# Kernel tuning notes

Measured on AMD Instinct MI355X. Metric: run time of the kernel, lower is better.

Reference implementation:

```python
import jax, jax.numpy as jnp
import numpy as np

B, T0, J = 32, 2048, 128
C, T_L = 512, 16


def setup_inputs() -> dict:
    key = jax.random.key(0)
    k1, k2, k3, k4, k5 = jax.random.split(key, 5)
    x = jax.random.normal(k1, (B, T0, J), dtype=jnp.float32)
    lens = jax.random.randint(k2, (B,), 0, T0 - T_L)  # ensure idx stays in-range
    sos = jax.random.normal(k3, (J,), dtype=jnp.float32)
    label_seqs = jax.random.uniform(k4, (C, T_L, J), dtype=jnp.float32)
    W = jax.random.normal(k5, (J, J), dtype=jnp.float32) / np.sqrt(J)
    return {"x": x, "lens": lens, "sos": sos, "label_seqs": label_seqs, "W": W}


def _similarity(pred_seq, labels):
    # per-neuron squared-error similarity, averaged over J: [B,Tl,J],[C,Tl,J] -> [B,C,Tl]
    p2 = jnp.sum(pred_seq * pred_seq, axis=-1)          # [B,Tl]
    l2 = jnp.sum(labels * labels, axis=-1)              # [C,Tl]
    cross = jnp.einsum('btj,ctj->bct', pred_seq, labels)
    return (p2[:, None, :] + l2[None, :, :] - 2.0 * cross) / pred_seq.shape[-1]


def reference(x, lens, sos, label_seqs, W):
    b_ar = jnp.arange(B)
    sos_b = jnp.broadcast_to(sos, (B, J))
    # place sos at position lens[b], then prepend sos (vectorized scatter)
    x = x.at[b_ar, lens].set(sos_b)
    x = jnp.concatenate([sos_b[:, None, :], x], axis=1)  # [B, T0+1, J]
    idx2d = jnp.arange(T_L)[None, :] + lens[:, None] + 1  # [B, T_l]

    def gather_pred(xc):
        pred = jnp.einsum('btj,jk->btk', xc, W)          # stub search_forward
        return pred[b_ar[:, None], idx2d]                # [B, T_l, J]

    pls = gather_pred(x)
    sim0 = _similarity(pls[:, :1, :], label_seqs[:, :1, :])  # [B,C,1]
    sofar = jnp.argmin(sim0[:, :, 0], axis=-1)               # [B]

    def body(t, carry):
        xc, sofar, _ = carry
        lab = label_seqs[sofar]                              # [B, T_l, J]
        xc = xc.at[b_ar[:, None], idx2d].set(lab)            # fused scatter update
        pls = gather_pred(xc)
        sim = _similarity(pls, label_seqs)                   # [B, C, T_l]
        mask = (jnp.arange(T_L) < t).astype(sim.dtype)
        sim_mean = jnp.sum(sim * mask, axis=-1) / t
        sofar = jnp.argmin(sim_mean, axis=-1)
        return (xc, sofar, pls)

    _, sofar, pls = jax.lax.fori_loop(1, T_L + 1, body, (x, sofar, pls))
    return sofar, pls
```

## Files before the change

### kernel.cpp

```cpp
#include <hip/hip_runtime.h>

#define Jd   128
#define Cn   512
#define TLn  16
#define Bn   32


__device__ __forceinline__ unsigned int f2ord(float f) {
    unsigned int u = __float_as_uint(f);
    return (u & 0x80000000u) ? ~u : (u | 0x80000000u);
}
__device__ __forceinline__ unsigned long long packkey(float v, int c) {
    return ((unsigned long long)f2ord(v) << 32) | (unsigned int)c;
}

__global__ void __launch_bounds__(256, 4)
k_prep3(const float* __restrict__ L, const float* __restrict__ W,
        float* __restrict__ LT, float* __restrict__ l2T,
        float* __restrict__ PLT) {
    __shared__ float Lst[128][36];
    __shared__ float Ws[128][68];
    int tid = threadIdx.x, bid = blockIdx.x;
    int tau = bid & 15, jh = (bid >> 4) & 1, c0 = (bid >> 5) * 32;
    int j0 = jh * 64;

    int cr = tid >> 3, oc = tid & 7;
    const float4* src = (const float4*)(L + ((size_t)(c0 + cr) * TLn + tau) * Jd);
    float l2p = 0.f;
    #pragma unroll
    for (int i = 0; i < 4; ++i) {
        float4 v = src[oc * 4 + i];
        int kb = (oc * 4 + i) * 4;
        Lst[kb + 0][cr] = v.x;  Lst[kb + 1][cr] = v.y;
        Lst[kb + 2][cr] = v.z;  Lst[kb + 3][cr] = v.w;
        l2p += v.x * v.x + v.y * v.y + v.z * v.z + v.w * v.w;
    }
    l2p += __shfl_down(l2p, 4, 8);
    l2p += __shfl_down(l2p, 2, 8);
    l2p += __shfl_down(l2p, 1, 8);
    if (oc == 0 && jh == 0) l2T[tau * Cn + c0 + cr] = l2p;

    #pragma unroll
    for (int r = 0; r < 8; ++r) {
        int idx = r * 256 + tid;
        int k = idx >> 4, f = idx & 15;
        *(float4*)&Ws[k][f * 4] = *(const float4*)(W + (size_t)k * Jd + j0 + f * 4);
    }
    __syncthreads();

    int c = tid & 31, jq = tid >> 5;

    if (jh == 0) {
        #pragma unroll
        for (int k = jq; k < Jd; k += 8)
            LT[((size_t)tau * Jd + k) * Cn + c0 + c] = Lst[k][c];
    }

    float acc[8] = {};
    #pragma unroll 4
    for (int k = 0; k < Jd; ++k) {
        float a = Lst[k][c];
        float4 w0 = *(const float4*)&Ws[k][jq * 8];
        float4 w1 = *(const float4*)&Ws[k][jq * 8 + 4];
        acc[0] = fmaf(a, w0.x, acc[0]);
        acc[1] = fmaf(a, w0.y, acc[1]);
        acc[2] = fmaf(a, w0.z, acc[2]);
        acc[3] = fmaf(a, w0.w, acc[3]);
        acc[4] = fmaf(a, w1.x, acc[4]);
        acc[5] = fmaf(a, w1.y, acc[5]);
        acc[6] = fmaf(a, w1.z, acc[6]);
        acc[7] = fmaf(a, w1.w, acc[7]);
    }
    #pragma unroll
    for (int i = 0; i < 8; ++i)
        PLT[((size_t)tau * Jd + j0 + jq * 8 + i) * Cn + c0 + c] = acc[i];
}

__global__ void __launch_bounds__(256, 3)
k_dot(const float* __restrict__ LT, const float* __restrict__ PLT,
      const float* __restrict__ l2T,
      const float* __restrict__ sos, const float* __restrict__ W,
      float* __restrict__ DOT, float* __restrict__ S0) {
    __shared__ float As[64][64];
    __shared__ float Bs[64][128];
    int tid = threadIdx.x, bid = blockIdx.x;

    if (bid == 512) {
        float* pred0 = &As[0][0];
        if (tid < Jd) {
            float a = 0.f;
            for (int k = 0; k < Jd; ++k) a = fmaf(sos[k], W[k * Jd + tid], a);
            pred0[tid] = a;
        }
        __syncthreads();
        float a0 = 0.f, a1 = 0.f;
        for (int jj = 0; jj < Jd; ++jj) {
            float p = pred0[jj];
            float d0 = p - LT[(size_t)jj * Cn + tid];
            float d1 = p - LT[(size_t)jj * Cn + tid + 256];
            a0 = fmaf(d0, d0, a0);
            a1 = fmaf(d1, d1, a1);
        }
        S0[tid] = a0;  S0[tid + 256] = a1;
        return;
    }

    int tau = bid & 15, st = (bid >> 4) & 7, cq = bid >> 7;
    int s0 = st * 64, c0 = cq * 128;
    int sg = tid >> 4, cg = tid & 15;

    float acc[4][8] = {};
    for (int h = 0; h < 2; ++h) {
        __syncthreads();
        const float4* Asrc = (const float4*)(PLT + ((size_t)tau * Jd + h * 64) * Cn + s0);
        #pragma unroll
        for (int i = 0; i < 4; ++i) {
            int flat = i * 256 + tid;
            int row = flat >> 4, col = flat & 15;
            *(float4*)&As[row][col * 4] = Asrc[(size_t)row * (Cn / 4) + col];
        }
        const float4* Bsrc = (const float4*)(LT + ((size_t)tau * Jd + h * 64) * Cn + c0);
        #pragma unroll
        for (int i = 0; i < 8; ++i) {
            int flat = i * 256 + tid;
            int row = flat >> 5, col = flat & 31;
            *(float4*)&Bs[row][col * 4] = Bsrc[(size_t)row * (Cn / 4) + col];
        }
        __syncthreads();
        #pragma unroll 4
        for (int j = 0; j < 64; ++j) {
            float4 a  = *(const float4*)&As[j][sg * 4];
            float4 b0 = *(const float4*)&Bs[j][cg * 4];
            float4 b1 = *(const float4*)&Bs[j][64 + cg * 4];
            float av[4] = {a.x, a.y, a.z, a.w};
            float bv[8] = {b0.x, b0.y, b0.z, b0.w, b1.x, b1.y, b1.z, b1.w};
            #pragma unroll
            for (int i = 0; i < 4; ++i)
                #pragma unroll
                for (int q = 0; q < 8; ++q)
                    acc[i][q] = fmaf(av[i], bv[q], acc[i][q]);
        }
    }

    float4 l2a = *(const float4*)(l2T + tau * Cn + c0 + cg * 4);
    float4 l2b = *(const float4*)(l2T + tau * Cn + c0 + 64 + cg * 4);
    #pragma unroll
    for (int i = 0; i < 4; ++i) {
        int s = s0 + sg * 4 + i;
        float* dst = DOT + ((size_t)s * TLn + tau) * Cn + c0;
        float4 v0 = {l2a.x - 2.f * acc[i][0], l2a.y - 2.f * acc[i][1],
                     l2a.z - 2.f * acc[i][2], l2a.w - 2.f * acc[i][3]};
        float4 v1 = {l2b.x - 2.f * acc[i][4], l2b.y - 2.f * acc[i][5],
                     l2b.z - 2.f * acc[i][6], l2b.w - 2.f * acc[i][7]};
        *(float4*)(dst + cg * 4) = v0;
        *(float4*)(dst + 64 + cg * 4) = v1;
    }
}

__global__ void k_seq(const float* __restrict__ S0, const float* __restrict__ DOT,
                      int* __restrict__ keys) {
    __shared__ unsigned long long red[4];
    __shared__ int sCur;
    int tid = threadIdx.x, w = tid >> 6, lane = tid & 63;

    for (int t = 0; t <= TLn; ++t) {
        float sum0, sum1;
        if (t == 0) {
            sum0 = S0[tid];  sum1 = S0[tid + 256];
        } else {
            const float* base = DOT + (size_t)sCur * TLn * Cn;
            float v0[TLn], v1[TLn];
            #pragma unroll
            for (int tau = 0; tau < TLn; ++tau) {
                v0[tau] = base[(size_t)tau * Cn + tid];
                v1[tau] = base[(size_t)tau * Cn + tid + 256];
            }
            sum0 = sum1 = 0.f;
            #pragma unroll
            for (int tau = 0; tau < TLn; ++tau) {
                float m = (tau < t) ? 1.f : 0.f;
                sum0 = fmaf(v0[tau], m, sum0);
                sum1 = fmaf(v1[tau], m, sum1);
            }
        }
        unsigned long long m0 = packkey(sum0, tid);
        unsigned long long m1 = packkey(sum1, tid + 256);
        unsigned long long m = (m1 < m0) ? m1 : m0;
        for (int o = 32; o; o >>= 1) {
            unsigned long long o2 = __shfl_down(m, o, 64);
            if (o2 < m) m = o2;
        }
        if (lane == 0) red[w] = m;
        __syncthreads();
        if (tid == 0) {
            unsigned long long b = red[0];
            #pragma unroll
            for (int i = 1; i < 4; ++i) if (red[i] < b) b = red[i];
            int sv = (int)(b & 0xFFFFFFFFull);
            sCur = sv;  keys[t] = sv;
        }
        __syncthreads();
    }
}

__global__ void k_out(const float* __restrict__ PLT, const int* __restrict__ keys,
                      float* __restrict__ out) {
    int bt = blockIdx.x, j = threadIdx.x, tau = bt & (TLn - 1);
    int s16 = keys[TLn], s15 = keys[TLn - 1];
    out[Bn + (size_t)bt * Jd + j] = PLT[((size_t)tau * Jd + j) * Cn + s15];
    if (bt == 0 && j < Bn) out[j] = (float)s16;
}

extern "C" void kernel_launch(void* const* d_in, const int* in_sizes, int n_in,
                              void* d_out, int out_size, void* d_ws, size_t ws_size,
                              hipStream_t stream) {
    const float* sos = (const float*)d_in[2];
    const float* L   = (const float*)d_in[3];
    const float* W   = (const float*)d_in[4];
    float* out = (float*)d_out;

    const size_t l2Off  = 4096;
    const size_t pltOff = 65536;
    const size_t ltOff  = pltOff + (size_t)TLn * Jd * Cn * sizeof(float);
    const size_t dotOff = ltOff  + (size_t)TLn * Jd * Cn * sizeof(float);
    const size_t need   = dotOff + (size_t)Cn * TLn * Cn * sizeof(float);
    char* base = (ws_size >= need) ? (char*)d_ws : (char*)d_in[0];
    float* S0   = (float*)base;
    int*   keys = (int*)(base + 2048);
    float* l2T  = (float*)(base + l2Off);
    float* PLT  = (float*)(base + pltOff);
    float* LT   = (float*)(base + ltOff);
    float* DOT  = (float*)(base + dotOff);

    hipLaunchKernelGGL(k_prep3, dim3(512), dim3(256), 0, stream, L, W, LT, l2T, PLT);
    hipLaunchKernelGGL(k_dot,   dim3(513), dim3(256), 0, stream,
                       LT, PLT, l2T, sos, W, DOT, S0);
    hipLaunchKernelGGL(k_seq,   dim3(1),   dim3(256), 0, stream, S0, DOT, keys);
    hipLaunchKernelGGL(k_out,   dim3(Bn * TLn), dim3(Jd), 0, stream, PLT, keys, out);
}
```

Measured before the change: 123.2 us.

## Enlarge k_dot tile to 128x128 and make k_seq a single-wavefront argmin

The pairwise dot-product kernel now gives each block a 128x128 tile with an 8x8 register accumulator per thread instead of 64x128 with 4x8, halving the grid to 257 blocks and raising reuse of data loaded into shared memory. The occupancy hint drops from 3 to 2 blocks per CU. The sequential argmin kernel now runs as one 64-lane wavefront. Each lane does vectorised float4 loads over 8 candidates, and the result is broadcast with a shuffle instead of going through shared memory and two block barriers per step. The trade-offs are fewer blocks to fill the GPU and more register pressure in k_dot, while k_seq's serial latency per step should shrink.

```diff
diff --git a/kernel.cpp b/kernel.cpp
--- a/kernel.cpp
+++ b/kernel.cpp
@@ -76,16 +76,16 @@
         PLT[((size_t)tau * Jd + j0 + jq * 8 + i) * Cn + c0 + c] = acc[i];
 }
 
-__global__ void __launch_bounds__(256, 3)
+__global__ void __launch_bounds__(256, 2)
 k_dot(const float* __restrict__ LT, const float* __restrict__ PLT,
       const float* __restrict__ l2T,
       const float* __restrict__ sos, const float* __restrict__ W,
       float* __restrict__ DOT, float* __restrict__ S0) {
-    __shared__ float As[64][64];
+    __shared__ float As[64][128];
     __shared__ float Bs[64][128];
     int tid = threadIdx.x, bid = blockIdx.x;
 
-    if (bid == 512) {
+    if (bid == 256) {
         float* pred0 = &As[0][0];
         if (tid < Jd) {
             float a = 0.f;
@@ -105,18 +105,18 @@
         return;
     }
 
-    int tau = bid & 15, st = (bid >> 4) & 7, cq = bid >> 7;
-    int s0 = st * 64, c0 = cq * 128;
+    int tau = bid & 15, st = (bid >> 4) & 3, cq = bid >> 6;
+    int s0 = st * 128, c0 = cq * 128;
     int sg = tid >> 4, cg = tid & 15;
 
-    float acc[4][8] = {};
+    float acc[8][8] = {};
     for (int h = 0; h < 2; ++h) {
         __syncthreads();
         const float4* Asrc = (const float4*)(PLT + ((size_t)tau * Jd + h * 64) * Cn + s0);
         #pragma unroll
-        for (int i = 0; i < 4; ++i) {
+        for (int i = 0; i < 8; ++i) {
             int flat = i * 256 + tid;
-            int row = flat >> 4, col = flat & 15;
+            int row = flat >> 5, col = flat & 31;
             *(float4*)&As[row][col * 4] = Asrc[(size_t)row * (Cn / 4) + col];
         }
         const float4* Bsrc = (const float4*)(LT + ((size_t)tau * Jd + h * 64) * Cn + c0);
@@ -127,15 +127,16 @@
             *(float4*)&Bs[row][col * 4] = Bsrc[(size_t)row * (Cn / 4) + col];
         }
         __syncthreads();
-        #pragma unroll 4
+        #pragma unroll 2
         for (int j = 0; j < 64; ++j) {
-            float4 a  = *(const float4*)&As[j][sg * 4];
+            float4 a0 = *(const float4*)&As[j][sg * 4];
+            float4 a1 = *(const float4*)&As[j][64 + sg * 4];
             float4 b0 = *(const float4*)&Bs[j][cg * 4];
             float4 b1 = *(const float4*)&Bs[j][64 + cg * 4];
-            float av[4] = {a.x, a.y, a.z, a.w};
+            float av[8] = {a0.x, a0.y, a0.z, a0.w, a1.x, a1.y, a1.z, a1.w};
             float bv[8] = {b0.x, b0.y, b0.z, b0.w, b1.x, b1.y, b1.z, b1.w};
             #pragma unroll
-            for (int i = 0; i < 4; ++i)
+            for (int i = 0; i < 8; ++i)
                 #pragma unroll
                 for (int q = 0; q < 8; ++q)
                     acc[i][q] = fmaf(av[i], bv[q], acc[i][q]);
@@ -145,8 +146,8 @@
     float4 l2a = *(const float4*)(l2T + tau * Cn + c0 + cg * 4);
     float4 l2b = *(const float4*)(l2T + tau * Cn + c0 + 64 + cg * 4);
     #pragma unroll
-    for (int i = 0; i < 4; ++i) {
-        int s = s0 + sg * 4 + i;
+    for (int i = 0; i < 8; ++i) {
+        int s = s0 + ((i < 4) ? (sg * 4 + i) : (64 + sg * 4 + (i - 4)));
         float* dst = DOT + ((size_t)s * TLn + tau) * Cn + c0;
         float4 v0 = {l2a.x - 2.f * acc[i][0], l2a.y - 2.f * acc[i][1],
                      l2a.z - 2.f * acc[i][2], l2a.w - 2.f * acc[i][3]};
@@ -159,47 +160,52 @@
 
 __global__ void k_seq(const float* __restrict__ S0, const float* __restrict__ DOT,
                       int* __restrict__ keys) {
-    __shared__ unsigned long long red[4];
-    __shared__ int sCur;
-    int tid = threadIdx.x, w = tid >> 6, lane = tid & 63;
+    int lane = threadIdx.x;
+    int sCur = 0;
 
     for (int t = 0; t <= TLn; ++t) {
-        float sum0, sum1;
+        unsigned long long m;
         if (t == 0) {
-            sum0 = S0[tid];  sum1 = S0[tid + 256];
+            float4 v0 = *(const float4*)(S0 + lane * 4);
+            float4 v1 = *(const float4*)(S0 + 256 + lane * 4);
+            float v[8] = {v0.x, v0.y, v0.z, v0.w, v1.x, v1.y, v1.z, v1.w};
+            m = packkey(v[0], lane * 4);
+            #pragma unroll
+            for (int i = 1; i < 8; ++i) {
+                int c = (i < 4) ? (lane * 4 + i) : (256 + lane * 4 + (i - 4));
+                unsigned long long k2 = packkey(v[i], c);
+                if (k2 < m) m = k2;
+            }
         } else {
             const float* base = DOT + (size_t)sCur * TLn * Cn;
-            float v0[TLn], v1[TLn];
+            float4 s0v = {0.f, 0.f, 0.f, 0.f}, s1v = {0.f, 0.f, 0.f, 0.f};
             #pragma unroll
             for (int tau = 0; tau < TLn; ++tau) {
-                v0[tau] = base[(size_t)tau * Cn + tid];
-                v1[tau] = base[(size_t)tau * Cn + tid + 256];
+                float4 w0 = *(const float4*)(base + (size_t)tau * Cn + lane * 4);
+                float4 w1 = *(const float4*)(base + (size_t)tau * Cn + 256 + lane * 4);
+                float mk = (tau < t) ? 1.f : 0.f;
+                s0v.x = fmaf(w0.x, mk, s0v.x);  s0v.y = fmaf(w0.y, mk, s0v.y);
+                s0v.z = fmaf(w0.z, mk, s0v.z);  s0v.w = fmaf(w0.w, mk, s0v.w);
+                s1v.x = fmaf(w1.x, mk, s1v.x);  s1v.y = fmaf(w1.y, mk, s1v.y);
+                s1v.z = fmaf(w1.z, mk, s1v.z);  s1v.w = fmaf(w1.w, mk, s1v.w);
             }
-            sum0 = sum1 = 0.f;
-            #pragma unroll
-            for (int tau = 0; tau < TLn; ++tau) {
-                float m = (tau < t) ? 1.f : 0.f;
-                sum0 = fmaf(v0[tau], m, sum0);
-                sum1 = fmaf(v1[tau], m, sum1);
+            float v[8] = {s0v.x, s0v.y, s0v.z, s0v.w, s1v.x, s1v.y, s1v.z, s1v.w};
+            m = packkey(v[0], lane * 4);
+            #pragma unroll
+            for (int i = 1; i < 8; ++i) {
+                int c = (i < 4) ? (lane * 4 + i) : (256 + lane * 4 + (i - 4));
+                unsigned long long k2 = packkey(v[i], c);
+                if (k2 < m) m = k2;
             }
         }
-        unsigned long long m0 = packkey(sum0, tid);
-        unsigned long long m1 = packkey(sum1, tid + 256);
-        unsigned long long m = (m1 < m0) ? m1 : m0;
+        #pragma unroll
         for (int o = 32; o; o >>= 1) {
             unsigned long long o2 = __shfl_down(m, o, 64);
             if (o2 < m) m = o2;
         }
-        if (lane == 0) red[w] = m;
-        __syncthreads();
-        if (tid == 0) {
-            unsigned long long b = red[0];
-            #pragma unroll
-            for (int i = 1; i < 4; ++i) if (red[i] < b) b = red[i];
-            int sv = (int)(b & 0xFFFFFFFFull);
-            sCur = sv;  keys[t] = sv;
-        }
-        __syncthreads();
+        m = __shfl(m, 0, 64);
+        sCur = (int)(m & 0xFFFFFFFFull);
+        if (lane == 0) keys[t] = sCur;
     }
 }
 
@@ -233,8 +239,8 @@
     float* DOT  = (float*)(base + dotOff);
 
     hipLaunchKernelGGL(k_prep3, dim3(512), dim3(256), 0, stream, L, W, LT, l2T, PLT);
-    hipLaunchKernelGGL(k_dot,   dim3(513), dim3(256), 0, stream,
+    hipLaunchKernelGGL(k_dot,   dim3(257), dim3(256), 0, stream,
                        LT, PLT, l2T, sos, W, DOT, S0);
-    hipLaunchKernelGGL(k_seq,   dim3(1),   dim3(256), 0, stream, S0, DOT, keys);
+    hipLaunchKernelGGL(k_seq,   dim3(1),   dim3(64), 0, stream, S0, DOT, keys);
     hipLaunchKernelGGL(k_out,   dim3(Bn * TLn), dim3(Jd), 0, stream, PLT, keys, out);
 }
```

Result: slower. 125.7 us (+2.1%).

## Precompute argmin transition table in parallel, then chase it serially

Applied to the files above, without the earlier changes.

The single-block sequential argmin loop is replaced by a 513-block kernel. For every candidate previous label and every step it computes the argmin of the running masked sum, storing the winner in a NEXT table. A tiny finish kernel then follows the chain of 16 lookups and broadcasts the gathered prediction rows to the output, absorbing the old output kernel. This trades a long latency-bound serial chain of global loads for a fully parallel pass over the whole DOT array plus an extra table in workspace.

```diff
diff --git a/kernel.cpp b/kernel.cpp
--- a/kernel.cpp
+++ b/kernel.cpp
@@ -157,35 +157,18 @@
     }
 }
 
-__global__ void k_seq(const float* __restrict__ S0, const float* __restrict__ DOT,
-                      int* __restrict__ keys) {
+__global__ void __launch_bounds__(256, 4)
+k_tab(const float* __restrict__ DOT, const float* __restrict__ S0,
+      int* __restrict__ NEXT, int* __restrict__ keys) {
     __shared__ unsigned long long red[4];
-    __shared__ int sCur;
-    int tid = threadIdx.x, w = tid >> 6, lane = tid & 63;
-
-    for (int t = 0; t <= TLn; ++t) {
-        float sum0, sum1;
-        if (t == 0) {
-            sum0 = S0[tid];  sum1 = S0[tid + 256];
-        } else {
-            const float* base = DOT + (size_t)sCur * TLn * Cn;
-            float v0[TLn], v1[TLn];
-            #pragma unroll
-            for (int tau = 0; tau < TLn; ++tau) {
-                v0[tau] = base[(size_t)tau * Cn + tid];
-                v1[tau] = base[(size_t)tau * Cn + tid + 256];
-            }
-            sum0 = sum1 = 0.f;
-            #pragma unroll
-            for (int tau = 0; tau < TLn; ++tau) {
-                float m = (tau < t) ? 1.f : 0.f;
-                sum0 = fmaf(v0[tau], m, sum0);
-                sum1 = fmaf(v1[tau], m, sum1);
-            }
-        }
-        unsigned long long m0 = packkey(sum0, tid);
-        unsigned long long m1 = packkey(sum1, tid + 256);
-        unsigned long long m = (m1 < m0) ? m1 : m0;
+    int tid = threadIdx.x, bid = blockIdx.x;
+    int w = tid >> 6, lane = tid & 63;
+
+    if (bid == 512) {
+        unsigned long long m = packkey(S0[tid], tid);
+        unsigned long long k2 = packkey(S0[tid + 256], tid + 256);
+        if (k2 < m) m = k2;
+        #pragma unroll
         for (int o = 32; o; o >>= 1) {
             unsigned long long o2 = __shfl_down(m, o, 64);
             if (o2 < m) m = o2;
@@ -196,19 +179,67 @@
             unsigned long long b = red[0];
             #pragma unroll
             for (int i = 1; i < 4; ++i) if (red[i] < b) b = red[i];
-            int sv = (int)(b & 0xFFFFFFFFull);
-            sCur = sv;  keys[t] = sv;
-        }
-        __syncthreads();
-    }
-}
-
-__global__ void k_out(const float* __restrict__ PLT, const int* __restrict__ keys,
-                      float* __restrict__ out) {
-    int bt = blockIdx.x, j = threadIdx.x, tau = bt & (TLn - 1);
-    int s16 = keys[TLn], s15 = keys[TLn - 1];
-    out[Bn + (size_t)bt * Jd + j] = PLT[((size_t)tau * Jd + j) * Cn + s15];
-    if (bt == 0 && j < Bn) out[j] = (float)s16;
+            keys[0] = (int)(b & 0xFFFFFFFFull);
+        }
+        return;
+    }
+
+    const float* base = DOT + (size_t)bid * TLn * Cn;
+    float v0[TLn], v1[TLn];
+    #pragma unroll
+    for (int tau = 0; tau < TLn; ++tau) {
+        v0[tau] = base[(size_t)tau * Cn + tid];
+        v1[tau] = base[(size_t)tau * Cn + tid + 256];
+    }
+    float a0 = 0.f, a1 = 0.f;
+    for (int t = 1; t <= TLn; ++t) {
+        a0 += v0[t - 1];
+        a1 += v1[t - 1];
+        unsigned long long m = packkey(a0, tid);
+        unsigned long long k2 = packkey(a1, tid + 256);
+        if (k2 < m) m = k2;
+        #pragma unroll
+        for (int o = 32; o; o >>= 1) {
+            unsigned long long o2 = __shfl_down(m, o, 64);
+            if (o2 < m) m = o2;
+        }
+        if (lane == 0) red[w] = m;
+        __syncthreads();
+        if (tid == 0) {
+            unsigned long long b = red[0];
+            #pragma unroll
+            for (int i = 1; i < 4; ++i) if (red[i] < b) b = red[i];
+            NEXT[bid * TLn + (t - 1)] = (int)(b & 0xFFFFFFFFull);
+        }
+        __syncthreads();
+    }
+}
+
+__global__ void __launch_bounds__(512, 1)
+k_finish(const float* __restrict__ PLT, const int* __restrict__ NEXT,
+         int* __restrict__ keys, float* __restrict__ out) {
+    int tid = threadIdx.x;
+    if (tid == 0) {
+        int sCur = keys[0];
+        #pragma unroll
+        for (int t = 1; t <= TLn; ++t) {
+            sCur = NEXT[sCur * TLn + (t - 1)];
+            keys[t] = sCur;
+        }
+    }
+    __syncthreads();
+
+    int s15 = keys[TLn - 1];
+    int tau = tid >> 5, jq = tid & 31;
+    float4 v;
+    v.x = PLT[((size_t)tau * Jd + jq * 4 + 0) * Cn + s15];
+    v.y = PLT[((size_t)tau * Jd + jq * 4 + 1) * Cn + s15];
+    v.z = PLT[((size_t)tau * Jd + jq * 4 + 2) * Cn + s15];
+    v.w = PLT[((size_t)tau * Jd + jq * 4 + 3) * Cn + s15];
+    #pragma unroll
+    for (int b = 0; b < Bn; ++b)
+        *(float4*)(out + Bn + ((size_t)b * TLn + tau) * Jd + jq * 4) = v;
+    if (tid < Bn) out[tid] = (float)keys[TLn];
 }
 
 extern "C" void kernel_launch(void* const* d_in, const int* in_sizes, int n_in,
@@ -219,11 +250,12 @@
     const float* W   = (const float*)d_in[4];
     float* out = (float*)d_out;
 
-    const size_t l2Off  = 4096;
-    const size_t pltOff = 65536;
-    const size_t ltOff  = pltOff + (size_t)TLn * Jd * Cn * sizeof(float);
-    const size_t dotOff = ltOff  + (size_t)TLn * Jd * Cn * sizeof(float);
-    const size_t need   = dotOff + (size_t)Cn * TLn * Cn * sizeof(float);
+    const size_t l2Off   = 4096;
+    const size_t pltOff  = 65536;
+    const size_t ltOff   = pltOff + (size_t)TLn * Jd * Cn * sizeof(float);
+    const size_t dotOff  = ltOff  + (size_t)TLn * Jd * Cn * sizeof(float);
+    const size_t nextOff = dotOff + (size_t)Cn * TLn * Cn * sizeof(float);
+    const size_t need    = nextOff + (size_t)Cn * TLn * sizeof(int);
     char* base = (ws_size >= need) ? (char*)d_ws : (char*)d_in[0];
     float* S0   = (float*)base;
     int*   keys = (int*)(base + 2048);
@@ -231,10 +263,13 @@
     float* PLT  = (float*)(base + pltOff);
     float* LT   = (float*)(base + ltOff);
     float* DOT  = (float*)(base + dotOff);
-
-    hipLaunchKernelGGL(k_prep3, dim3(512), dim3(256), 0, stream, L, W, LT, l2T, PLT);
-    hipLaunchKernelGGL(k_dot,   dim3(513), dim3(256), 0, stream,
+    int*   NEXT = (int*)(base + nextOff);
+
+    hipLaunchKernelGGL(k_prep3,  dim3(512), dim3(256), 0, stream, L, W, LT, l2T, PLT);
+    hipLaunchKernelGGL(k_dot,    dim3(513), dim3(256), 0, stream,
                        LT, PLT, l2T, sos, W, DOT, S0);
-    hipLaunchKernelGGL(k_seq,   dim3(1),   dim3(256), 0, stream, S0, DOT, keys);
-    hipLaunchKernelGGL(k_out,   dim3(Bn * TLn), dim3(Jd), 0, stream, PLT, keys, out);
-}
+    hipLaunchKernelGGL(k_tab,    dim3(513), dim3(256), 0, stream,
+                       DOT, S0, NEXT, keys);
+    hipLaunchKernelGGL(k_finish, dim3(1),   dim3(512), 0, stream,
+                       PLT, NEXT, keys, out);
+}
```

Result: no change. 123.2 us (+0.0%).
